# Kernel optimization log

Measured on AMD Instinct MI355X. Metric: run time of the kernel, lower is better.

Reference implementation:

```python
import jax, jax.numpy as jnp
import numpy as np

EPS = 1e-5

def _layernorm(x, w, b):
    mu = jnp.mean(x, axis=-1, keepdims=True)
    var = jnp.mean(jnp.square(x - mu), axis=-1, keepdims=True)
    return (x - mu) * jax.lax.rsqrt(var + EPS) * w + b

def setup_inputs() -> dict:
    key = jax.random.key(0)
    ks = jax.random.split(key, 8)
    B, N, C, D = 32, 1024, 4096, 64
    x = jax.random.normal(ks[0], (B, N, C), dtype=jnp.float32)
    gumbel = jax.random.gumbel(ks[1], (B, N, 2), dtype=jnp.float32)
    ln_w = jnp.ones((C,), jnp.float32)
    ln_b = jnp.zeros((C,), jnp.float32)
    w1 = jax.random.normal(ks[2], (C, D), dtype=jnp.float32) * 0.02
    b1 = jnp.zeros((D,), jnp.float32)
    w2 = jax.random.normal(ks[3], (D, 2), dtype=jnp.float32) * 0.02
    b2 = jnp.zeros((2,), jnp.float32)
    return {"x": x, "gumbel": gumbel, "ln_w": ln_w, "ln_b": ln_b,
            "w1": w1, "b1": b1, "w2": w2, "b2": b2}

def reference(x, gumbel, ln_w, ln_b, w1, b1, w2, b2):
    B, N, C = x.shape
    xn = _layernorm(x, ln_w, ln_b)
    local_x = xn[:, :, : C // 2]                      # [B, N, C/2]
    # policy is all-ones -> weighted mean over tokens
    global_x = jnp.mean(xn[:, :, C // 2:], axis=1, keepdims=True)  # [B, 1, C/2]
    feat = jnp.concatenate(
        [local_x, jnp.broadcast_to(global_x, local_x.shape)], axis=-1)  # [B, N, C]
    h = jax.nn.gelu(feat @ w1 + b1, approximate=False)  # [B, N, 64]
    logits = h @ w2 + b2                                # [B, N, 2]
    pred_score = jax.nn.log_softmax(logits, axis=-1)
    # gumbel-softmax (tau=1, hard=True) with straight-through estimator
    y_soft = jax.nn.softmax(pred_score + gumbel, axis=-1)
    hard = jax.nn.one_hot(jnp.argmax(y_soft, axis=-1), 2, dtype=y_soft.dtype)
    y = hard - jax.lax.stop_gradient(y_soft) + y_soft
    keep = y[:, :, 0]                                   # [B, N]
    # dense equivalent of masked_select/split: zero out dropped tokens
    return x * keep[:, :, None]
```

## Files before the change

### kernel.cpp

```cpp
#include <hip/hip_runtime.h>
#include <math.h>

#define B_   32
#define N_   1024
#define C_   4096
#define HC_  2048
#define D_   64
#define NT_  32768
#define KS_  4
#define KC_  (HC_ / KS_)
#define BKC_ 32

__device__ __forceinline__ float4 ld4(const float* p) {
    return *reinterpret_cast<const float4*>(p);
}

__global__ __launch_bounds__(256) void k3_fused(
        const float* __restrict__ x, const float* __restrict__ lnw,
        const float* __restrict__ w1, float* __restrict__ Pp,
        float* __restrict__ spq) {
    __shared__ float As[BKC_ * 128];
    __shared__ float Bsm[BKC_ * D_];

    const int t = threadIdx.x;
    const int mt = blockIdx.x & 255;
    const int ks = blockIdx.x >> 8;
    const int T0 = mt * 128;
    const int kbase = ks * KC_;
    const int rt = t & 31;
    const int dt = t >> 5;
    const int lrow = t >> 3;
    const int lq = t & 7;

    float acc[32];
#pragma unroll
    for (int i = 0; i < 32; ++i) acc[i] = 0.f;
    float sRow[4], qRow[4];
#pragma unroll
    for (int p = 0; p < 4; ++p) { sRow[p] = 0.f; qRow[p] = 0.f; }

    float4 xv[4];
    float4 wv1, wv2;
    float lw1, lw2;
    {
        const int k0 = kbase;
#pragma unroll
        for (int p = 0; p < 4; ++p)
            xv[p] = ld4(x + (size_t)(T0 + lrow + 32 * p) * C_ + k0 + lq * 4);
        const float4* s4 = reinterpret_cast<const float4*>(
            w1 + (size_t)k0 * D_);
        wv1 = s4[t]; wv2 = s4[256 + t];
        lw1 = lnw[k0 + (t >> 4)];
        lw2 = lnw[k0 + 16 + (t >> 4)];
    }

#pragma unroll 1
    for (int kc = 0; kc < KC_ / BKC_; ++kc) {
#pragma unroll
        for (int p = 0; p < 4; ++p) {
            const float4 v = xv[p];
            const int r = lrow + 32 * p;
            const int gq = r >> 2, rm = r & 3;
            const int kb = 4 * lq;
#pragma unroll
            for (int j = 0; j < 4; ++j) {
                const float c = (j == 0) ? v.x : (j == 1) ? v.y
                              : (j == 2) ? v.z : v.w;
                const int p5 = (5 * lq + j) & 31;
                As[(kb + j) * 128 + (((gq ^ p5) << 2) + rm)] = c;
            }
            sRow[p] += (v.x + v.y) + (v.z + v.w);
            qRow[p] = fmaf(v.x, v.x, fmaf(v.y, v.y,
                      fmaf(v.z, v.z, fmaf(v.w, v.w, qRow[p]))));
        }
        {
            float4 v1 = wv1, v2 = wv2;
            v1.x *= lw1; v1.y *= lw1; v1.z *= lw1; v1.w *= lw1;
            v2.x *= lw2; v2.y *= lw2; v2.z *= lw2; v2.w *= lw2;
            float4* b4 = reinterpret_cast<float4*>(Bsm);
            b4[t] = v1;
            b4[256 + t] = v2;
        }
        __syncthreads();
        if (kc + 1 < KC_ / BKC_) {
            const int k1 = kbase + (kc + 1) * BKC_;
#pragma unroll
            for (int p = 0; p < 4; ++p)
                xv[p] = ld4(x + (size_t)(T0 + lrow + 32 * p) * C_
                            + k1 + lq * 4);
            const float4* s4 = reinterpret_cast<const float4*>(
                w1 + (size_t)k1 * D_);
            wv1 = s4[t]; wv2 = s4[256 + t];
            lw1 = lnw[k1 + (t >> 4)];
            lw2 = lnw[k1 + 16 + (t >> 4)];
        }
#pragma unroll 8
        for (int k = 0; k < BKC_; ++k) {
            const int p5 = (5 * (k >> 2) + (k & 3)) & 31;
            const float4 a4 = *reinterpret_cast<const float4*>(
                As + k * 128 + ((rt ^ p5) << 2));
            const float* br = Bsm + k * D_ + dt * 8;
            const float4 b0 = ld4(br), b1v = ld4(br + 4);
            const float av[4] = {a4.x, a4.y, a4.z, a4.w};
            const float bv[8] = {b0.x, b0.y, b0.z, b0.w,
                                 b1v.x, b1v.y, b1v.z, b1v.w};
#pragma unroll
            for (int ri = 0; ri < 4; ++ri)
#pragma unroll
                for (int cj = 0; cj < 8; ++cj)
                    acc[ri * 8 + cj] =
                        fmaf(av[ri], bv[cj], acc[ri * 8 + cj]);
        }
        __syncthreads();
    }
#pragma unroll
    for (int ri = 0; ri < 4; ++ri) {
        float* dst = Pp + ((size_t)ks * NT_ + T0 + rt * 4 + ri) * D_ + dt * 8;
        *reinterpret_cast<float4*>(dst) = make_float4(
            acc[ri * 8 + 0], acc[ri * 8 + 1], acc[ri * 8 + 2],
            acc[ri * 8 + 3]);
        *reinterpret_cast<float4*>(dst + 4) = make_float4(
            acc[ri * 8 + 4], acc[ri * 8 + 5], acc[ri * 8 + 6],
            acc[ri * 8 + 7]);
    }
#pragma unroll
    for (int p = 0; p < 4; ++p) {
        float s = sRow[p], q = qRow[p];
        s += __shfl_xor(s, 1); q += __shfl_xor(q, 1);
        s += __shfl_xor(s, 2); q += __shfl_xor(q, 2);
        s += __shfl_xor(s, 4); q += __shfl_xor(q, 4);
        if (lq == 0) {
            const size_t r = (size_t)(T0 + lrow + 32 * p) * 8;
            spq[r + ks] = s;
            spq[r + 4 + ks] = q;
        }
    }
}

__global__ __launch_bounds__(256) void k1_upper(
        const float* __restrict__ x, const float* __restrict__ lnw,
        const float* __restrict__ lnb, const float* __restrict__ spq,
        float* __restrict__ muv, float* __restrict__ rsv,
        float* __restrict__ part) {
    __shared__ float sh[4][HC_];
    const int t = threadIdx.x;
    const int lane = t & 63, w = t >> 6;
    const int bid = blockIdx.x;
    const int b = bid >> 5;
    const int g = bid & 31;

    float4 wv[8], bv[8], gacc[8];
#pragma unroll
    for (int m = 0; m < 8; ++m) {
        wv[m] = ld4(lnw + HC_ + (m * 64 + lane) * 4);
        bv[m] = ld4(lnb + HC_ + (m * 64 + lane) * 4);
        gacc[m] = make_float4(0.f, 0.f, 0.f, 0.f);
    }

    for (int i = 0; i < 8; ++i) {
        const int tok = b * N_ + g * 32 + w * 8 + i;
        const float* row = x + (size_t)tok * C_ + HC_;
        float4 v[8];
        float s = 0.f, q = 0.f;
#pragma unroll
        for (int m = 0; m < 8; ++m) {
            v[m] = ld4(row + (m * 64 + lane) * 4);
            s += (v[m].x + v[m].y) + (v[m].z + v[m].w);
            q = fmaf(v[m].x, v[m].x, fmaf(v[m].y, v[m].y,
                fmaf(v[m].z, v[m].z, fmaf(v[m].w, v[m].w, q))));
        }
#pragma unroll
        for (int o = 1; o < 64; o <<= 1) {
            s += __shfl_xor(s, o);
            q += __shfl_xor(q, o);
        }
        const float4 s0 = ld4(spq + (size_t)tok * 8);
        const float4 q0 = ld4(spq + (size_t)tok * 8 + 4);
        const float S = s + (s0.x + s0.y) + (s0.z + s0.w);
        const float Q = q + (q0.x + q0.y) + (q0.z + q0.w);
        const float mu = S * (1.f / C_);
        const float rs = rsqrtf(Q * (1.f / C_) - mu * mu + 1e-5f);
        if (lane == 0) {
            muv[tok] = mu;
            rsv[tok] = rs;
        }
#pragma unroll
        for (int m = 0; m < 8; ++m) {
            gacc[m].x += (v[m].x - mu) * rs * wv[m].x + bv[m].x;
            gacc[m].y += (v[m].y - mu) * rs * wv[m].y + bv[m].y;
            gacc[m].z += (v[m].z - mu) * rs * wv[m].z + bv[m].z;
            gacc[m].w += (v[m].w - mu) * rs * wv[m].w + bv[m].w;
        }
    }
#pragma unroll
    for (int m = 0; m < 8; ++m)
        *reinterpret_cast<float4*>(&sh[w][(m * 64 + lane) * 4]) = gacc[m];
    __syncthreads();
    float* pp = part + (size_t)bid * HC_;
#pragma unroll
    for (int m = 0; m < 8; ++m) {
        const int j = (m * 64 + lane) * 4;
        const float4 a0 = ld4(&sh[0][j]);
        const float4 a1 = ld4(&sh[1][j]);
        const float4 a2 = ld4(&sh[2][j]);
        const float4 a3 = ld4(&sh[3][j]);
        float4 r;
        r.x = (a0.x + a1.x) + (a2.x + a3.x);
        r.y = (a0.y + a1.y) + (a2.y + a3.y);
        r.z = (a0.z + a1.z) + (a2.z + a3.z);
        r.w = (a0.w + a1.w) + (a2.w + a3.w);
        if (w == (m & 3))
            *reinterpret_cast<float4*>(pp + j) = r;
    }
}

__global__ __launch_bounds__(256) void k2a_part(
        const float* __restrict__ part, const float* __restrict__ w1,
        const float* __restrict__ lnw, const float* __restrict__ lnb,
        float* __restrict__ gpart, float* __restrict__ Wpart,
        float* __restrict__ Bpart) {
    __shared__ float Gs[256];
    __shared__ float red[512];
    const int t = threadIdx.x;
    const int d = t & 63, s = t >> 6;
    const int blk = blockIdx.x;
    if (blk < 256) {
        const int b = blk >> 3, jq = blk & 7;
        const int j = jq * 256 + t;
        float a = 0.f;
        for (int k = 0; k < 32; ++k)
            a += part[(size_t)(b * 32 + k) * HC_ + j];
        Gs[t] = a;
        __syncthreads();
        float acc = 0.f;
        const int j0 = jq * 256 + s * 64;
        for (int jj = 0; jj < 64; ++jj)
            acc = fmaf(Gs[s * 64 + jj],
                       w1[(size_t)(HC_ + j0 + jj) * D_ + d], acc);
        red[s * 64 + d] = acc;
        __syncthreads();
        if (s == 0)
            gpart[(size_t)blk * 64 + d] =
                red[d] + red[64 + d] + red[128 + d] + red[192 + d];
    } else {
        const int wq = blk - 256;
        const int c0 = wq * 256 + s * 64;
        float a = 0.f, c2 = 0.f;
        for (int c = c0; c < c0 + 64; ++c) {
            const float wvv = w1[(size_t)c * D_ + d];
            a = fmaf(lnw[c], wvv, a);
            c2 = fmaf(lnb[c], wvv, c2);
        }
        red[s * 64 + d] = a;
        red[256 + s * 64 + d] = c2;
        __syncthreads();
        if (s == 0) {
            Wpart[wq * 64 + d] =
                red[d] + red[64 + d] + red[128 + d] + red[192 + d];
            Bpart[wq * 64 + d] = red[256 + d] + red[320 + d]
                               + red[384 + d] + red[448 + d];
        }
    }
}

__global__ __launch_bounds__(64) void k2b_final(
        const float* __restrict__ gpart, const float* __restrict__ Wpart,
        const float* __restrict__ Bpart, float* __restrict__ gterm,
        float* __restrict__ W1s, float* __restrict__ Bs) {
    const int d = threadIdx.x;
    const int b = blockIdx.x;
    if (b < B_) {
        float a = 0.f;
#pragma unroll
        for (int q = 0; q < 8; ++q)
            a += gpart[(size_t)(b * 8 + q) * 64 + d];
        gterm[b * D_ + d] = a * (1.f / N_);
    } else {
        float a = 0.f, c2 = 0.f;
#pragma unroll
        for (int q = 0; q < 8; ++q) {
            a += Wpart[q * 64 + d];
            c2 += Bpart[q * 64 + d];
        }
        W1s[d] = a;
        Bs[d] = c2;
    }
}

__global__ __launch_bounds__(256) void k45_decide_mask(
        const float* __restrict__ Pp, const float* __restrict__ muv,
        const float* __restrict__ rsv, const float* __restrict__ gterm,
        const float* __restrict__ W1s, const float* __restrict__ Bs,
        const float* __restrict__ b1, const float* __restrict__ w2,
        const float* __restrict__ b2, const float* __restrict__ gum,
        const float* __restrict__ x, float* __restrict__ out) {
    const int t = threadIdx.x;
    const int lane = t & 63, w = t >> 6;
    const int token = blockIdx.x * 4 + w;
    const int b = token >> 10;

    const float2 gv = *reinterpret_cast<const float2*>(gum + token * 2);
    float p = 0.f;
#pragma unroll
    for (int s = 0; s < KS_; ++s)
        p += Pp[((size_t)s * NT_ + token) * D_ + lane];

    const float mu = muv[token], rs = rsv[token];
    float h = rs * (p - mu * W1s[lane]) + Bs[lane] + gterm[b * D_ + lane]
              + b1[lane];
    h = 0.5f * h * (1.f + erff(h * 0.70710678118654752f));
    const float2 w2v = *reinterpret_cast<const float2*>(w2 + lane * 2);
    float l0 = h * w2v.x;
    float l1 = h * w2v.y;
#pragma unroll
    for (int o = 1; o < 64; o <<= 1) {
        l0 += __shfl_xor(l0, o);
        l1 += __shfl_xor(l1, o);
    }
    const float z0 = l0 + b2[0] + gv.x;
    const float z1 = l1 + b2[1] + gv.y;

    float4* dst = reinterpret_cast<float4*>(out + (size_t)token * C_);
    if (z0 >= z1) {
        const float4* src =
            reinterpret_cast<const float4*>(x + (size_t)token * C_);
#pragma unroll
        for (int c = 0; c < 16; ++c)
            dst[c * 64 + lane] = src[c * 64 + lane];
    } else {
        const float4 z = make_float4(0.f, 0.f, 0.f, 0.f);
#pragma unroll
        for (int c = 0; c < 16; ++c)
            dst[c * 64 + lane] = z;
    }
}

extern "C" void kernel_launch(void* const* d_in, const int* in_sizes, int n_in,
                              void* d_out, int out_size, void* d_ws,
                              size_t ws_size, hipStream_t stream) {
    const float* x   = (const float*)d_in[0];
    const float* gum = (const float*)d_in[1];
    const float* lnw = (const float*)d_in[2];
    const float* lnb = (const float*)d_in[3];
    const float* w1  = (const float*)d_in[4];
    const float* b1  = (const float*)d_in[5];
    const float* w2  = (const float*)d_in[6];
    const float* b2  = (const float*)d_in[7];
    float* out = (float*)d_out;

    float* wsf   = (float*)d_ws;
    float* Pp    = wsf;
    float* muv   = Pp + (size_t)KS_ * NT_ * D_;
    float* rsv   = muv + NT_;
    float* part  = rsv + NT_;
    float* gterm = part + (size_t)1024 * HC_;
    float* W1s   = gterm + B_ * D_;
    float* Bs    = W1s + D_;
    float* spq   = Bs + D_;
    float* gpart = spq + (size_t)NT_ * 8;
    float* Wpart = gpart + 256 * 64;
    float* Bpart = Wpart + 8 * 64;

    k3_fused<<<KS_ * 256, 256, 0, stream>>>(x, lnw, w1, Pp, spq);
    k1_upper<<<1024, 256, 0, stream>>>(x, lnw, lnb, spq, muv, rsv, part);
    k2a_part<<<264, 256, 0, stream>>>(part, w1, lnw, lnb,
                                      gpart, Wpart, Bpart);
    k2b_final<<<33, 64, 0, stream>>>(gpart, Wpart, Bpart, gterm, W1s, Bs);
    k45_decide_mask<<<NT_ / 4, 256, 0, stream>>>(Pp, muv, rsv, gterm, W1s,
                                                 Bs, b1, w2, b2, gum, x, out);
}
```

Before: 398.1 us.

## Fuse lower-half GEMM and upper-half layernorm stats into one kernel per token tile

Result: faster. 370.8 us (-6.9%).

```diff
diff --git a/kernel.cpp b/kernel.cpp
--- a/kernel.cpp
+++ b/kernel.cpp
@@ -7,147 +7,121 @@
 #define HC_  2048
 #define D_   64
 #define NT_  32768
-#define KS_  4
-#define KC_  (HC_ / KS_)
 #define BKC_ 32
+#define NCH_ (HC_ / BKC_)
+#define AST_ 68
 
 __device__ __forceinline__ float4 ld4(const float* p) {
     return *reinterpret_cast<const float4*>(p);
 }
 
-__global__ __launch_bounds__(256) void k3_fused(
+__global__ __launch_bounds__(256) void mk1(
         const float* __restrict__ x, const float* __restrict__ lnw,
-        const float* __restrict__ w1, float* __restrict__ Pp,
-        float* __restrict__ spq) {
-    __shared__ float As[BKC_ * 128];
-    __shared__ float Bsm[BKC_ * D_];
+        const float* __restrict__ lnb, const float* __restrict__ w1,
+        float* __restrict__ Pp, float* __restrict__ muv,
+        float* __restrict__ rsv, float* __restrict__ part) {
+    __shared__ float smem[8704];
+    __shared__ float sLow[64], qLow[64];
+
+    float* As0 = smem;
+    float* As1 = smem + 2176;
+    float* Bs0 = smem + 4352;
+    float* Bs1 = smem + 6400;
 
     const int t = threadIdx.x;
-    const int mt = blockIdx.x & 255;
-    const int ks = blockIdx.x >> 8;
-    const int T0 = mt * 128;
-    const int kbase = ks * KC_;
-    const int rt = t & 31;
-    const int dt = t >> 5;
-    const int lrow = t >> 3;
-    const int lq = t & 7;
-
-    float acc[32];
-#pragma unroll
-    for (int i = 0; i < 32; ++i) acc[i] = 0.f;
-    float sRow[4], qRow[4];
-#pragma unroll
-    for (int p = 0; p < 4; ++p) { sRow[p] = 0.f; qRow[p] = 0.f; }
-
-    float4 xv[4];
-    float4 wv1, wv2;
+    const int tid = blockIdx.x;
+    const int T0 = tid * 64;
+    const int rt = t & 15;
+    const int dt = t >> 4;
+    const int row = t >> 2;
+    const int fq = t & 3;
+    const int lane = t & 63, w = t >> 6;
+
+    float acc[16];
+#pragma unroll
+    for (int i = 0; i < 16; ++i) acc[i] = 0.f;
+    float sR = 0.f, qR = 0.f;
+
+    float4 xv1, xv2, wv1, wv2;
     float lw1, lw2;
     {
-        const int k0 = kbase;
-#pragma unroll
-        for (int p = 0; p < 4; ++p)
-            xv[p] = ld4(x + (size_t)(T0 + lrow + 32 * p) * C_ + k0 + lq * 4);
-        const float4* s4 = reinterpret_cast<const float4*>(
-            w1 + (size_t)k0 * D_);
+        const float* rp = x + (size_t)(T0 + row) * C_;
+        xv1 = ld4(rp + fq * 4);
+        xv2 = ld4(rp + 16 + fq * 4);
+        const float4* s4 = reinterpret_cast<const float4*>(w1);
         wv1 = s4[t]; wv2 = s4[256 + t];
-        lw1 = lnw[k0 + (t >> 4)];
-        lw2 = lnw[k0 + 16 + (t >> 4)];
+        lw1 = lnw[t >> 4];
+        lw2 = lnw[16 + (t >> 4)];
     }
 
 #pragma unroll 1
-    for (int kc = 0; kc < KC_ / BKC_; ++kc) {
-#pragma unroll
-        for (int p = 0; p < 4; ++p) {
-            const float4 v = xv[p];
-            const int r = lrow + 32 * p;
-            const int gq = r >> 2, rm = r & 3;
-            const int kb = 4 * lq;
-#pragma unroll
-            for (int j = 0; j < 4; ++j) {
-                const float c = (j == 0) ? v.x : (j == 1) ? v.y
-                              : (j == 2) ? v.z : v.w;
-                const int p5 = (5 * lq + j) & 31;
-                As[(kb + j) * 128 + (((gq ^ p5) << 2) + rm)] = c;
-            }
-            sRow[p] += (v.x + v.y) + (v.z + v.w);
-            qRow[p] = fmaf(v.x, v.x, fmaf(v.y, v.y,
-                      fmaf(v.z, v.z, fmaf(v.w, v.w, qRow[p]))));
+    for (int c = 0; c < NCH_; ++c) {
+        float* Ab = (c & 1) ? As1 : As0;
+        float* Bb = (c & 1) ? Bs1 : Bs0;
+        {
+            const int kb1 = fq * 4, kb2 = 16 + fq * 4;
+            Ab[(kb1 + 0) * AST_ + row] = xv1.x;
+            Ab[(kb1 + 1) * AST_ + row] = xv1.y;
+            Ab[(kb1 + 2) * AST_ + row] = xv1.z;
+            Ab[(kb1 + 3) * AST_ + row] = xv1.w;
+            Ab[(kb2 + 0) * AST_ + row] = xv2.x;
+            Ab[(kb2 + 1) * AST_ + row] = xv2.y;
+            Ab[(kb2 + 2) * AST_ + row] = xv2.z;
+            Ab[(kb2 + 3) * AST_ + row] = xv2.w;
+            sR += ((xv1.x + xv1.y) + (xv1.z + xv1.w))
+                + ((xv2.x + xv2.y) + (xv2.z + xv2.w));
+            qR = fmaf(xv1.x, xv1.x, fmaf(xv1.y, xv1.y,
+                 fmaf(xv1.z, xv1.z, fmaf(xv1.w, xv1.w, qR))));
+            qR = fmaf(xv2.x, xv2.x, fmaf(xv2.y, xv2.y,
+                 fmaf(xv2.z, xv2.z, fmaf(xv2.w, xv2.w, qR))));
         }
         {
             float4 v1 = wv1, v2 = wv2;
             v1.x *= lw1; v1.y *= lw1; v1.z *= lw1; v1.w *= lw1;
             v2.x *= lw2; v2.y *= lw2; v2.z *= lw2; v2.w *= lw2;
-            float4* b4 = reinterpret_cast<float4*>(Bsm);
+            float4* b4 = reinterpret_cast<float4*>(Bb);
             b4[t] = v1;
             b4[256 + t] = v2;
         }
         __syncthreads();
-        if (kc + 1 < KC_ / BKC_) {
-            const int k1 = kbase + (kc + 1) * BKC_;
-#pragma unroll
-            for (int p = 0; p < 4; ++p)
-                xv[p] = ld4(x + (size_t)(T0 + lrow + 32 * p) * C_
-                            + k1 + lq * 4);
+        if (c + 1 < NCH_) {
+            const int k1 = (c + 1) * BKC_;
+            const float* rp = x + (size_t)(T0 + row) * C_ + k1;
+            xv1 = ld4(rp + fq * 4);
+            xv2 = ld4(rp + 16 + fq * 4);
             const float4* s4 = reinterpret_cast<const float4*>(
                 w1 + (size_t)k1 * D_);
             wv1 = s4[t]; wv2 = s4[256 + t];
             lw1 = lnw[k1 + (t >> 4)];
             lw2 = lnw[k1 + 16 + (t >> 4)];
         }
-#pragma unroll 8
+#pragma unroll
         for (int k = 0; k < BKC_; ++k) {
-            const int p5 = (5 * (k >> 2) + (k & 3)) & 31;
             const float4 a4 = *reinterpret_cast<const float4*>(
-                As + k * 128 + ((rt ^ p5) << 2));
-            const float* br = Bsm + k * D_ + dt * 8;
-            const float4 b0 = ld4(br), b1v = ld4(br + 4);
+                Ab + k * AST_ + rt * 4);
+            const float4 b4 = *reinterpret_cast<const float4*>(
+                Bb + k * 64 + dt * 4);
             const float av[4] = {a4.x, a4.y, a4.z, a4.w};
-            const float bv[8] = {b0.x, b0.y, b0.z, b0.w,
-                                 b1v.x, b1v.y, b1v.z, b1v.w};
+            const float bv[4] = {b4.x, b4.y, b4.z, b4.w};
 #pragma unroll
             for (int ri = 0; ri < 4; ++ri)
 #pragma unroll
-                for (int cj = 0; cj < 8; ++cj)
-                    acc[ri * 8 + cj] =
-                        fmaf(av[ri], bv[cj], acc[ri * 8 + cj]);
-        }
-        __syncthreads();
+                for (int cj = 0; cj < 4; ++cj)
+                    acc[ri * 4 + cj] =
+                        fmaf(av[ri], bv[cj], acc[ri * 4 + cj]);
+        }
     }
 #pragma unroll
     for (int ri = 0; ri < 4; ++ri) {
-        float* dst = Pp + ((size_t)ks * NT_ + T0 + rt * 4 + ri) * D_ + dt * 8;
+        float* dst = Pp + (size_t)(T0 + rt * 4 + ri) * D_ + dt * 4;
         *reinterpret_cast<float4*>(dst) = make_float4(
-            acc[ri * 8 + 0], acc[ri * 8 + 1], acc[ri * 8 + 2],
-            acc[ri * 8 + 3]);
-        *reinterpret_cast<float4*>(dst + 4) = make_float4(
-            acc[ri * 8 + 4], acc[ri * 8 + 5], acc[ri * 8 + 6],
-            acc[ri * 8 + 7]);
-    }
-#pragma unroll
-    for (int p = 0; p < 4; ++p) {
-        float s = sRow[p], q = qRow[p];
-        s += __shfl_xor(s, 1); q += __shfl_xor(q, 1);
-        s += __shfl_xor(s, 2); q += __shfl_xor(q, 2);
-        s += __shfl_xor(s, 4); q += __shfl_xor(q, 4);
-        if (lq == 0) {
-            const size_t r = (size_t)(T0 + lrow + 32 * p) * 8;
-            spq[r + ks] = s;
-            spq[r + 4 + ks] = q;
-        }
-    }
-}
-
-__global__ __launch_bounds__(256) void k1_upper(
-        const float* __restrict__ x, const float* __restrict__ lnw,
-        const float* __restrict__ lnb, const float* __restrict__ spq,
-        float* __restrict__ muv, float* __restrict__ rsv,
-        float* __restrict__ part) {
-    __shared__ float sh[4][HC_];
-    const int t = threadIdx.x;
-    const int lane = t & 63, w = t >> 6;
-    const int bid = blockIdx.x;
-    const int b = bid >> 5;
-    const int g = bid & 31;
+            acc[ri * 4 + 0], acc[ri * 4 + 1],
+            acc[ri * 4 + 2], acc[ri * 4 + 3]);
+    }
+    sR += __shfl_xor(sR, 1); qR += __shfl_xor(qR, 1);
+    sR += __shfl_xor(sR, 2); qR += __shfl_xor(qR, 2);
+    if (fq == 0) { sLow[row] = sR; qLow[row] = qR; }
+    __syncthreads();
 
     float4 wv[8], bv[8], gacc[8];
 #pragma unroll
@@ -156,15 +130,15 @@
         bv[m] = ld4(lnb + HC_ + (m * 64 + lane) * 4);
         gacc[m] = make_float4(0.f, 0.f, 0.f, 0.f);
     }
-
-    for (int i = 0; i < 8; ++i) {
-        const int tok = b * N_ + g * 32 + w * 8 + i;
-        const float* row = x + (size_t)tok * C_ + HC_;
+    for (int i = 0; i < 16; ++i) {
+        const int r = w * 16 + i;
+        const int tok = T0 + r;
+        const float* rowp = x + (size_t)tok * C_ + HC_;
         float4 v[8];
         float s = 0.f, q = 0.f;
 #pragma unroll
         for (int m = 0; m < 8; ++m) {
-            v[m] = ld4(row + (m * 64 + lane) * 4);
+            v[m] = ld4(rowp + (m * 64 + lane) * 4);
             s += (v[m].x + v[m].y) + (v[m].z + v[m].w);
             q = fmaf(v[m].x, v[m].x, fmaf(v[m].y, v[m].y,
                 fmaf(v[m].z, v[m].z, fmaf(v[m].w, v[m].w, q))));
@@ -174,10 +148,8 @@
             s += __shfl_xor(s, o);
             q += __shfl_xor(q, o);
         }
-        const float4 s0 = ld4(spq + (size_t)tok * 8);
-        const float4 q0 = ld4(spq + (size_t)tok * 8 + 4);
-        const float S = s + (s0.x + s0.y) + (s0.z + s0.w);
-        const float Q = q + (q0.x + q0.y) + (q0.z + q0.w);
+        const float S = s + sLow[r];
+        const float Q = q + qLow[r];
         const float mu = S * (1.f / C_);
         const float rs = rsqrtf(Q * (1.f / C_) - mu * mu + 1e-5f);
         if (lane == 0) {
@@ -192,11 +164,12 @@
             gacc[m].w += (v[m].w - mu) * rs * wv[m].w + bv[m].w;
         }
     }
+    float (*sh)[HC_] = reinterpret_cast<float(*)[HC_]>(smem);
 #pragma unroll
     for (int m = 0; m < 8; ++m)
         *reinterpret_cast<float4*>(&sh[w][(m * 64 + lane) * 4]) = gacc[m];
     __syncthreads();
-    float* pp = part + (size_t)bid * HC_;
+    float* pp = part + (size_t)tid * HC_;
 #pragma unroll
     for (int m = 0; m < 8; ++m) {
         const int j = (m * 64 + lane) * 4;
@@ -228,8 +201,8 @@
         const int b = blk >> 3, jq = blk & 7;
         const int j = jq * 256 + t;
         float a = 0.f;
-        for (int k = 0; k < 32; ++k)
-            a += part[(size_t)(b * 32 + k) * HC_ + j];
+        for (int k = 0; k < 16; ++k)
+            a += part[(size_t)(b * 16 + k) * HC_ + j];
         Gs[t] = a;
         __syncthreads();
         float acc = 0.f;
@@ -263,34 +236,10 @@
     }
 }
 
-__global__ __launch_bounds__(64) void k2b_final(
-        const float* __restrict__ gpart, const float* __restrict__ Wpart,
-        const float* __restrict__ Bpart, float* __restrict__ gterm,
-        float* __restrict__ W1s, float* __restrict__ Bs) {
-    const int d = threadIdx.x;
-    const int b = blockIdx.x;
-    if (b < B_) {
-        float a = 0.f;
-#pragma unroll
-        for (int q = 0; q < 8; ++q)
-            a += gpart[(size_t)(b * 8 + q) * 64 + d];
-        gterm[b * D_ + d] = a * (1.f / N_);
-    } else {
-        float a = 0.f, c2 = 0.f;
-#pragma unroll
-        for (int q = 0; q < 8; ++q) {
-            a += Wpart[q * 64 + d];
-            c2 += Bpart[q * 64 + d];
-        }
-        W1s[d] = a;
-        Bs[d] = c2;
-    }
-}
-
 __global__ __launch_bounds__(256) void k45_decide_mask(
         const float* __restrict__ Pp, const float* __restrict__ muv,
-        const float* __restrict__ rsv, const float* __restrict__ gterm,
-        const float* __restrict__ W1s, const float* __restrict__ Bs,
+        const float* __restrict__ rsv, const float* __restrict__ gpart,
+        const float* __restrict__ Wpart, const float* __restrict__ Bpart,
         const float* __restrict__ b1, const float* __restrict__ w2,
         const float* __restrict__ b2, const float* __restrict__ gum,
         const float* __restrict__ x, float* __restrict__ out) {
@@ -299,15 +248,19 @@
     const int token = blockIdx.x * 4 + w;
     const int b = token >> 10;
 
+    float W1 = 0.f, Bsv = 0.f, gt = 0.f;
+#pragma unroll
+    for (int q = 0; q < 8; ++q) {
+        W1 += Wpart[q * 64 + lane];
+        Bsv += Bpart[q * 64 + lane];
+        gt += gpart[(size_t)(b * 8 + q) * 64 + lane];
+    }
+    gt *= (1.f / N_);
+
     const float2 gv = *reinterpret_cast<const float2*>(gum + token * 2);
-    float p = 0.f;
-#pragma unroll
-    for (int s = 0; s < KS_; ++s)
-        p += Pp[((size_t)s * NT_ + token) * D_ + lane];
-
+    const float p = Pp[(size_t)token * D_ + lane];
     const float mu = muv[token], rs = rsv[token];
-    float h = rs * (p - mu * W1s[lane]) + Bs[lane] + gterm[b * D_ + lane]
-              + b1[lane];
+    float h = rs * (p - mu * W1) + Bsv + gt + b1[lane];
     h = 0.5f * h * (1.f + erff(h * 0.70710678118654752f));
     const float2 w2v = *reinterpret_cast<const float2*>(w2 + lane * 2);
     float l0 = h * w2v.x;
@@ -350,22 +303,17 @@
 
     float* wsf   = (float*)d_ws;
     float* Pp    = wsf;
-    float* muv   = Pp + (size_t)KS_ * NT_ * D_;
+    float* muv   = Pp + (size_t)NT_ * D_;
     float* rsv   = muv + NT_;
     float* part  = rsv + NT_;
-    float* gterm = part + (size_t)1024 * HC_;
-    float* W1s   = gterm + B_ * D_;
-    float* Bs    = W1s + D_;
-    float* spq   = Bs + D_;
-    float* gpart = spq + (size_t)NT_ * 8;
+    float* gpart = part + (size_t)512 * HC_;
     float* Wpart = gpart + 256 * 64;
     float* Bpart = Wpart + 8 * 64;
 
-    k3_fused<<<KS_ * 256, 256, 0, stream>>>(x, lnw, w1, Pp, spq);
-    k1_upper<<<1024, 256, 0, stream>>>(x, lnw, lnb, spq, muv, rsv, part);
+    mk1<<<512, 256, 0, stream>>>(x, lnw, lnb, w1, Pp, muv, rsv, part);
     k2a_part<<<264, 256, 0, stream>>>(part, w1, lnw, lnb,
                                       gpart, Wpart, Bpart);
-    k2b_final<<<33, 64, 0, stream>>>(gpart, Wpart, Bpart, gterm, W1s, Bs);
-    k45_decide_mask<<<NT_ / 4, 256, 0, stream>>>(Pp, muv, rsv, gterm, W1s,
-                                                 Bs, b1, w2, b2, gum, x, out);
-}
+    k45_decide_mask<<<NT_ / 4, 256, 0, stream>>>(Pp, muv, rsv, gpart,
+                                                 Wpart, Bpart, b1, w2, b2,
+                                                 gum, x, out);
+}
```
